# Kernel tuning notes

Hardware: AMD Instinct MI355X
Metric: run time of the kernel (lower is better)

Reference implementation:

```python
import jax, jax.numpy as jnp
import numpy as np

K0 = 0.7978845608028654  # sqrt(2/pi)
C1 = 0.044715

def _gelu_tanh(x):
    # tanh-approx GELU, matching the Triton kernel's math
    return 0.5 * x * (1.0 + jnp.tanh(K0 * (x + C1 * x * x * x)))

def setup_inputs() -> dict:
    key = jax.random.key(0)
    k1, k2, k3 = jax.random.split(key, 3)
    B, C_in, H, W = 32, 64, 128, 128
    C_out, KH = 128, 3
    x = jax.random.normal(k1, (B, C_in, H, W), dtype=jnp.float32)
    weight = jax.random.normal(k2, (C_out, C_in, KH, KH), dtype=jnp.float32)
    bias = jax.random.normal(k3, (C_out,), dtype=jnp.float32)
    return {"x": x, "weight": weight, "bias": bias}

def reference(x, weight, bias):
    # Valid conv2d, stride 1 (NCHW, OIHW)
    y = jax.lax.conv_general_dilated(
        x, weight,
        window_strides=(1, 1), padding="VALID",
        dimension_numbers=("NCHW", "OIHW", "NCHW"))
    y = y + bias[None, :, None, None]
    y = _gelu_tanh(y)
    # global average pool over spatial dims -> [B, C_out]
    return jnp.mean(y, axis=(2, 3))
```

## Files before the change

kernel.cpp:

```cpp
#include <hip/hip_runtime.h>
#include <cstdint>
#include <cstddef>

#define GK0 0.7978845608028654f
#define GC1 0.044715f

typedef __attribute__((ext_vector_type(8))) short short8;
typedef __attribute__((ext_vector_type(4))) float floatx4;

__device__ __forceinline__ unsigned short f2bf(float f) {
  union { float f; unsigned int u; } v; v.f = f;
  unsigned int r = v.u + 0x7fffu + ((v.u >> 16) & 1u);
  return (unsigned short)(r >> 16);
}

__device__ __forceinline__ void gl_lds16(const unsigned short* g, unsigned short* l) {
  __builtin_amdgcn_global_load_lds(
      (const __attribute__((address_space(1))) unsigned int*)g,
      (__attribute__((address_space(3))) unsigned int*)l, 16, 0, 0);
}

__global__ void k_wt(const float* __restrict__ w, unsigned short* __restrict__ wt,
                     float* __restrict__ out) {
  if (blockIdx.x == 0) {
    for (int i = threadIdx.x; i < 32 * 128; i += 256) out[i] = 0.0f;
  }
  int t = blockIdx.x * 256 + threadIdx.x;
  if (t >= 128 * 64 * 9) return;
  int co = t / 576; int r = t - co * 576; int ci = r / 9; int khw = r - ci * 9;
  wt[(khw * 128 + co) * 64 + ci] = f2bf(w[t]);
}

__global__ __launch_bounds__(256) void k_xt(const float* __restrict__ x,
                                            unsigned short* __restrict__ xb) {
  __shared__ float tile[64 * 132];
  const int tid = threadIdx.x, lane = tid & 63, wv = tid >> 6;
  const int b = blockIdx.y, h0 = blockIdx.x * 4;
  const int w4 = lane & 31, cih = lane >> 5;

  for (int r = 0; r < 4; r++) {
    const int h = h0 + r;
#pragma unroll
    for (int j = 0; j < 8; j++) {
      const int ci = wv * 16 + 2 * j + cih;
      float4 f = *(const float4*)(x + ((size_t)(b * 64 + ci) * 128 + h) * 128 + 4 * w4);
      *(float4*)&tile[ci * 132 + 4 * w4] = f;
    }
    __syncthreads();
    unsigned short* orow = xb + ((size_t)b * 128 + h) * 8192;
    const int oct = tid & 7, wlo = tid >> 3;
#pragma unroll
    for (int it = 0; it < 4; it++) {
      const int w = wlo + 32 * it;
      short8 v;
#pragma unroll
      for (int j = 0; j < 8; j++) v[j] = (short)f2bf(tile[(8 * oct + j) * 132 + w]);
      *(short8*)(orow + w * 64 + oct * 8) = v;
    }
    __syncthreads();
  }
}

__global__ __launch_bounds__(256, 3) void k_conv(
    const unsigned short* __restrict__ xb, const unsigned short* __restrict__ wt,
    const float* __restrict__ bias, float* __restrict__ out) {
  __shared__ __align__(16) unsigned short As[8192];
  __shared__ __align__(16) unsigned short Bs[8192];
  const int tid = threadIdx.x, lane = tid & 63, wv = tid >> 6;
  const int w0 = blockIdx.x * 64, h0 = blockIdx.y * 2, b = blockIdx.z;
  const int wm = wv & 1, wn = wv >> 1;
  const int m = lane & 15, q = lane >> 4;

  floatx4 acc[4][4];
#pragma unroll
  for (int i = 0; i < 4; i++)
#pragma unroll
    for (int j = 0; j < 4; j++) acc[i][j] = (floatx4){0.f, 0.f, 0.f, 0.f};

  const unsigned short* xbb = xb + (size_t)b * 128 * 8192;
  const int rh = wv >> 1, cc0 = (wv & 1) * 4;

#pragma unroll
  for (int khw = 0; khw < 9; khw++) {
    const int kh = khw / 3, kw = khw - 3 * kh;
    const unsigned short* ag = wt + khw * 8192 + wv * 2048 + lane * 8;
    unsigned short* al = As + wv * 2048;
#pragma unroll
    for (int i = 0; i < 4; i++) gl_lds16(ag + i * 512, al + i * 512);
    const unsigned short* bg =
        xbb + ((size_t)(h0 + rh + kh) * 128 + w0 + kw) * 64 + cc0 * 512 + lane * 8;
    unsigned short* bl = Bs + (rh * 8 + cc0) * 512;
#pragma unroll
    for (int i = 0; i < 4; i++) gl_lds16(bg + i * 512, bl + i * 512);
    __syncthreads();

#pragma unroll
    for (int half = 0; half < 2; half++) {
      short8 a[4], bf[4];
#pragma unroll
      for (int mt = 0; mt < 4; mt++)
        a[mt] = *(const short8*)&As[(wm * 64 + mt * 16 + m) * 64 + half * 32 + q * 8];
#pragma unroll
      for (int nt = 0; nt < 4; nt++)
        bf[nt] = *(const short8*)&Bs[(wn * 64 + nt * 16 + m) * 64 + half * 32 + q * 8];
#pragma unroll
      for (int mt = 0; mt < 4; mt++)
#pragma unroll
        for (int nt = 0; nt < 4; nt++)
          acc[mt][nt] = __builtin_amdgcn_mfma_f32_16x16x32_bf16(a[mt], bf[nt], acc[mt][nt], 0, 0, 0);
    }
    __syncthreads();
  }

  const float inv_area = 1.0f / (126.0f * 126.0f);
  float* orow = out + b * 128;
#pragma unroll
  for (int mt = 0; mt < 4; mt++)
#pragma unroll
    for (int r2 = 0; r2 < 4; r2++) {
      const int co = wm * 64 + mt * 16 + q * 4 + r2;
      const float bv = bias[co];
      float s = 0.f;
#pragma unroll
      for (int nt = 0; nt < 4; nt++) {
        float y = acc[mt][nt][r2] + bv;
        float u = GK0 * (y + GC1 * y * y * y);
        float e = __expf(-2.0f * u);
        float g = y * __builtin_amdgcn_rcpf(1.0f + e);
        if (w0 + nt * 16 + m < 126) s += g;
      }
#pragma unroll
      for (int d = 1; d < 16; d <<= 1) s += __shfl_xor(s, d, 64);
      if (m == 0) atomicAdd(&orow[co], s * inv_area);
    }
}

extern "C" void kernel_launch(void* const* d_in, const int* in_sizes, int n_in,
                              void* d_out, int out_size, void* d_ws, size_t ws_size,
                              hipStream_t stream) {
  const float* x    = (const float*)d_in[0];
  const float* w    = (const float*)d_in[1];
  const float* bias = (const float*)d_in[2];
  float* out = (float*)d_out;

  const size_t xb_elems = (size_t)32 * 128 * 8192;
  unsigned short* xbuf = (unsigned short*)d_ws;
  unsigned short* wbuf = xbuf + xb_elems + 2048;
  if (ws_size < xb_elems * 2 + 4096 + (size_t)9 * 128 * 64 * 2) return;

  k_wt<<<288, 256, 0, stream>>>(w, wbuf, out);
  k_xt<<<dim3(32, 32), 256, 0, stream>>>(x, xbuf);
  k_conv<<<dim3(2, 63, 32), 256, 0, stream>>>(xbuf, wbuf, bias, out);
}
```

Baseline: 380.6 us.

## Double-buffer conv LDS stages with XOR swizzle and merge prep kernels

```diff
diff --git a/kernel.cpp b/kernel.cpp
--- a/kernel.cpp
+++ b/kernel.cpp
@@ -20,56 +20,64 @@
       (__attribute__((address_space(3))) unsigned int*)l, 16, 0, 0);
 }
 
-__global__ void k_wt(const float* __restrict__ w, unsigned short* __restrict__ wt,
-                     float* __restrict__ out) {
-  if (blockIdx.x == 0) {
-    for (int i = threadIdx.x; i < 32 * 128; i += 256) out[i] = 0.0f;
-  }
-  int t = blockIdx.x * 256 + threadIdx.x;
-  if (t >= 128 * 64 * 9) return;
-  int co = t / 576; int r = t - co * 576; int ci = r / 9; int khw = r - ci * 9;
-  wt[(khw * 128 + co) * 64 + ci] = f2bf(w[t]);
-}
-
-__global__ __launch_bounds__(256) void k_xt(const float* __restrict__ x,
-                                            unsigned short* __restrict__ xb) {
-  __shared__ float tile[64 * 132];
-  const int tid = threadIdx.x, lane = tid & 63, wv = tid >> 6;
-  const int b = blockIdx.y, h0 = blockIdx.x * 4;
-  const int w4 = lane & 31, cih = lane >> 5;
-
-  for (int r = 0; r < 4; r++) {
-    const int h = h0 + r;
+__global__ __launch_bounds__(256) void k_prep(
+    const float* __restrict__ x, const float* __restrict__ w,
+    unsigned short* __restrict__ xb, unsigned short* __restrict__ wt,
+    float* __restrict__ out) {
+  const int bx = blockIdx.x;
+  if (bx < 2048) {
+    const int b = bx >> 6, h = ((bx & 63) << 1) + (threadIdx.x >> 7);
+    const int wcol = threadIdx.x & 127;
+    const float* src = x + (size_t)b * 64 * 16384 + (size_t)h * 128 + wcol;
+    unsigned short* dst = xb + (((size_t)b * 128 + h) * 128 + wcol) * 64;
 #pragma unroll
-    for (int j = 0; j < 8; j++) {
-      const int ci = wv * 16 + 2 * j + cih;
-      float4 f = *(const float4*)(x + ((size_t)(b * 64 + ci) * 128 + h) * 128 + 4 * w4);
-      *(float4*)&tile[ci * 132 + 4 * w4] = f;
-    }
-    __syncthreads();
-    unsigned short* orow = xb + ((size_t)b * 128 + h) * 8192;
-    const int oct = tid & 7, wlo = tid >> 3;
+    for (int ch = 0; ch < 8; ch++) {
+      float f[8];
 #pragma unroll
-    for (int it = 0; it < 4; it++) {
-      const int w = wlo + 32 * it;
+      for (int j = 0; j < 8; j++) f[j] = src[(size_t)(8 * ch + j) * 16384];
       short8 v;
 #pragma unroll
-      for (int j = 0; j < 8; j++) v[j] = (short)f2bf(tile[(8 * oct + j) * 132 + w]);
-      *(short8*)(orow + w * 64 + oct * 8) = v;
+      for (int j = 0; j < 8; j++) v[j] = (short)f2bf(f[j]);
+      *(short8*)(dst + ch * 8) = v;
     }
-    __syncthreads();
+  } else {
+    if (bx == 2048) {
+      for (int i = threadIdx.x; i < 32 * 128; i += 256) out[i] = 0.0f;
+    }
+    const int t = (bx - 2048) * 256 + threadIdx.x;
+    if (t < 128 * 64 * 9) {
+      int co = t / 576; int r = t - co * 576; int ci = r / 9; int khw = r - ci * 9;
+      wt[(khw * 128 + co) * 64 + ci] = f2bf(w[t]);
+    }
   }
 }
 
-__global__ __launch_bounds__(256, 3) void k_conv(
+__global__ __launch_bounds__(256, 2) void k_conv(
     const unsigned short* __restrict__ xb, const unsigned short* __restrict__ wt,
     const float* __restrict__ bias, float* __restrict__ out) {
-  __shared__ __align__(16) unsigned short As[8192];
-  __shared__ __align__(16) unsigned short Bs[8192];
+  __shared__ __align__(16) unsigned short xs[2][16384];
   const int tid = threadIdx.x, lane = tid & 63, wv = tid >> 6;
   const int w0 = blockIdx.x * 64, h0 = blockIdx.y * 2, b = blockIdx.z;
   const int wm = wv & 1, wn = wv >> 1;
   const int m = lane & 15, q = lane >> 4;
+
+  const int lr = lane >> 3, lco = ((lane & 7) ^ lr) << 3;
+  const unsigned short* aln = wt + (32 * wv + lr) * 64 + lco;
+  const unsigned short* xbb = xb + (size_t)b * 128 * 8192;
+  const int srh = wv >> 1;
+  const size_t bln = (size_t)(32 * (wv & 1) + lr) * 64 + lco;
+
+#define STAGE(khw_, bufi_)                                                        \
+  {                                                                               \
+    const int kh_ = (khw_) / 3, kw_ = (khw_)-3 * kh_;                             \
+    unsigned short* Al = &xs[bufi_][0] + wv * 2048;                               \
+    const unsigned short* Ag = aln + (khw_)*8192;                                 \
+    _Pragma("unroll") for (int i = 0; i < 4; i++) gl_lds16(Ag + i * 512, Al + i * 512); \
+    unsigned short* Bl = &xs[bufi_][8192] + wv * 2048;                            \
+    const unsigned short* Bg =                                                    \
+        xbb + ((size_t)(h0 + srh + kh_) * 128 + w0 + kw_) * 64 + bln;             \
+    _Pragma("unroll") for (int i = 0; i < 4; i++) gl_lds16(Bg + i * 512, Bl + i * 512); \
+  }
 
   floatx4 acc[4][4];
 #pragma unroll
@@ -77,39 +85,30 @@
 #pragma unroll
     for (int j = 0; j < 4; j++) acc[i][j] = (floatx4){0.f, 0.f, 0.f, 0.f};
 
-  const unsigned short* xbb = xb + (size_t)b * 128 * 8192;
-  const int rh = wv >> 1, cc0 = (wv & 1) * 4;
+  STAGE(0, 0);
 
 #pragma unroll
-  for (int khw = 0; khw < 9; khw++) {
-    const int kh = khw / 3, kw = khw - 3 * kh;
-    const unsigned short* ag = wt + khw * 8192 + wv * 2048 + lane * 8;
-    unsigned short* al = As + wv * 2048;
-#pragma unroll
-    for (int i = 0; i < 4; i++) gl_lds16(ag + i * 512, al + i * 512);
-    const unsigned short* bg =
-        xbb + ((size_t)(h0 + rh + kh) * 128 + w0 + kw) * 64 + cc0 * 512 + lane * 8;
-    unsigned short* bl = Bs + (rh * 8 + cc0) * 512;
-#pragma unroll
-    for (int i = 0; i < 4; i++) gl_lds16(bg + i * 512, bl + i * 512);
+  for (int kk = 0; kk < 9; kk++) {
     __syncthreads();
-
+    if (kk < 8) STAGE(kk + 1, (kk + 1) & 1);
+    const unsigned short* As = &xs[kk & 1][0];
+    const unsigned short* Bs = &xs[kk & 1][8192];
 #pragma unroll
     for (int half = 0; half < 2; half++) {
+      const int coff = (((half << 2) | q) ^ (m & 7)) << 3;
       short8 a[4], bf[4];
 #pragma unroll
       for (int mt = 0; mt < 4; mt++)
-        a[mt] = *(const short8*)&As[(wm * 64 + mt * 16 + m) * 64 + half * 32 + q * 8];
+        a[mt] = *(const short8*)&As[(wm * 64 + mt * 16 + m) * 64 + coff];
 #pragma unroll
       for (int nt = 0; nt < 4; nt++)
-        bf[nt] = *(const short8*)&Bs[(wn * 64 + nt * 16 + m) * 64 + half * 32 + q * 8];
+        bf[nt] = *(const short8*)&Bs[(wn * 64 + nt * 16 + m) * 64 + coff];
 #pragma unroll
       for (int mt = 0; mt < 4; mt++)
 #pragma unroll
         for (int nt = 0; nt < 4; nt++)
           acc[mt][nt] = __builtin_amdgcn_mfma_f32_16x16x32_bf16(a[mt], bf[nt], acc[mt][nt], 0, 0, 0);
     }
-    __syncthreads();
   }
 
   const float inv_area = 1.0f / (126.0f * 126.0f);
@@ -145,10 +144,9 @@
 
   const size_t xb_elems = (size_t)32 * 128 * 8192;
   unsigned short* xbuf = (unsigned short*)d_ws;
-  unsigned short* wbuf = xbuf + xb_elems + 2048;
-  if (ws_size < xb_elems * 2 + 4096 + (size_t)9 * 128 * 64 * 2) return;
+  unsigned short* wbuf = xbuf + xb_elems + 8192;
+  if (ws_size < xb_elems * 2 + 16384 + (size_t)9 * 128 * 64 * 2) return;
 
-  k_wt<<<288, 256, 0, stream>>>(w, wbuf, out);
-  k_xt<<<dim3(32, 32), 256, 0, stream>>>(x, xbuf);
+  k_prep<<<2336, 256, 0, stream>>>(x, w, xbuf, wbuf, out);
   k_conv<<<dim3(2, 63, 32), 256, 0, stream>>>(xbuf, wbuf, bias, out);
 }
```

New measurement: 397.1 us. +4.3%, slower.
